# Kernel tuning notes

Hardware: AMD Instinct MI355X
Metric: run time of the kernel (lower is better)

The kernel has to match this reference:

```python
import jax, jax.numpy as jnp
import numpy as np

NBINS_PIX = 256   # uint8 pixel values
NBINS_MEAN = 512  # neighbor mean fits in [0, 408] for side=1


def setup_inputs() -> dict:
    key = jax.random.key(0)
    # uniform [0,1) so x.max() < 1.0 branch (x*255 quantization) is taken, as in the source
    x = jax.random.uniform(key, (64, 1024, 1024), dtype=jnp.float32)
    return {"x": x}


def reference(x):
    H, W = x.shape[-2:]
    x = jax.lax.stop_gradient(x)  # mirrors .clone().detach()
    xf = x.reshape(-1, H, W)
    B = xf.shape[0]
    # quantize: (x*255).to(uint8) if max<1 else x.to(uint8); uint8 cast truncates
    scale = jnp.where(jnp.max(xf) < 1.0, jnp.float32(255.0), jnp.float32(1.0))
    xq = (xf * scale).astype(jnp.uint8).astype(jnp.float32)
    xi = xq.astype(jnp.int32)

    # zero-padded 8-neighbor sum (3x3 window minus center), side=1
    xp = jnp.pad(xi, ((0, 0), (1, 1), (1, 1)))
    nb = jnp.zeros_like(xi)
    for dh in range(3):
        for dw in range(3):
            if dh == 1 and dw == 1:
                continue
            nb = nb + xp[:, dh:dh + H, dw:dw + W]

    # Faithful replication of the source's normalization: the original indexes
    # mean_nb[a, b] where dim0 is the BATCH dim and dim1 is the row dim, so the
    # divisor depends on (batch, row) and broadcasts over columns.
    # t=0: num=3 at 4 (batch,row) corners; then num->5 for edges and interior.
    D = jnp.ones((B, H), dtype=jnp.float32)
    D = D.at[0, 0].set(3.0).at[-1, 0].set(3.0).at[0, -1].set(3.0).at[-1, -1].set(3.0)
    D = D.at[1:-1, 0].set(5.0).at[1:-1, -1].set(5.0)
    D = D.at[0, 1:-1].set(5.0).at[-1, 1:-1].set(5.0)
    D = D.at[1:-1, 1:-1].set(5.0)
    mean_nb = nb.astype(jnp.float32) / D[:, :, None]
    mean_i = mean_nb.astype(jnp.int32)  # trunc toward zero, values >= 0

    # joint (pixel, mean) histogram per image -> entropy, matches unique+counts
    codes = xi * NBINS_MEAN + mean_i  # in [0, 256*512)

    def hist_entropy(c):
        counts = jnp.zeros(NBINS_PIX * NBINS_MEAN, jnp.float32).at[c.reshape(-1)].add(1.0)
        p = counts / (H * W)
        safe = jnp.where(p > 0, p, 1.0)
        return jnp.sum(jnp.where(p > 0, -p * jnp.log2(safe), 0.0))

    ent = jax.vmap(hist_entropy)(codes)  # [B]
    return jnp.mean(ent)
```

## Files before the change

kernel.cpp:

```cpp
#include <hip/hip_runtime.h>

#define IMG_H 1024
#define IMG_W 1024
#define NPIX  (IMG_H * IMG_W)
#define NBINS (256 * 512)
#define TILE  64
#define LW    (TILE + 2)

#define MEANS  428
#define HBINS  (256 * MEANS)
#define HWORDS (HBINS / 4)
#define QUADS  4
#define QROWS  (IMG_H / QUADS)

__global__ __launch_bounds__(1024) void fused_hist_kernel(const float* __restrict__ x,
                                                          unsigned int* __restrict__ partials,
                                                          int B) {
    __shared__ unsigned int h[HWORDS];

    const int blk  = blockIdx.x;
    const int b    = blk >> 2;
    const int quad = blk & 3;
    const int tid  = threadIdx.x;

    for (int i = tid; i < HWORDS; i += 1024) h[i] = 0u;
    __syncthreads();

    const float* img = x + (size_t)b * NPIX;
    const int c0    = (tid & 255) * 4;
    const int strip = tid >> 8;
    const int rs    = quad * QROWS + strip * (QROWS / 4);
    const int re    = rs + QROWS / 4;
    const bool bEdge = (b == 0) || (b == B - 1);

    auto loadraw = [&](int r, float4& f, float& fl, float& fr) {
        if ((unsigned)r < IMG_H) {
            const float* row = img + r * IMG_W;
            f  = *(const float4*)(row + c0);
            fl = (c0 > 0) ? row[c0 - 1] : 0.0f;
            fr = (c0 + 4 < IMG_W) ? row[c0 + 4] : 0.0f;
        } else { f = make_float4(0.f, 0.f, 0.f, 0.f); fl = 0.f; fr = 0.f; }
    };
    auto quant6 = [&](const float4& f, float fl, float fr, int q[6]) {
        q[0] = (int)(fl  * 255.0f);
        q[1] = (int)(f.x * 255.0f);
        q[2] = (int)(f.y * 255.0f);
        q[3] = (int)(f.z * 255.0f);
        q[4] = (int)(f.w * 255.0f);
        q[5] = (int)(fr  * 255.0f);
    };

    int hA[4], hB[4], qB[4];
    {
        float4 f; float fl, fr; loadraw(rs - 1, f, fl, fr);
        int q[6]; quant6(f, fl, fr, q);
#pragma unroll
        for (int i = 0; i < 4; ++i) hA[i] = q[i] + q[i + 1] + q[i + 2];
    }
    {
        float4 f; float fl, fr; loadraw(rs, f, fl, fr);
        int q[6]; quant6(f, fl, fr, q);
#pragma unroll
        for (int i = 0; i < 4; ++i) { hB[i] = q[i] + q[i + 1] + q[i + 2]; qB[i] = q[i + 1]; }
    }
    float4 pf; float pfl, pfr; loadraw(rs + 1, pf, pfl, pfr);

    for (int r = rs; r < re; ++r) {
        float4 cf = pf; float cfl = pfl, cfr = pfr;
        loadraw(r + 2, pf, pfl, pfr);

        int q[6]; quant6(cf, cfl, cfr, q);
        int hC[4];
#pragma unroll
        for (int i = 0; i < 4; ++i) hC[i] = q[i] + q[i + 1] + q[i + 2];

        const bool corner = bEdge && (r == 0 || r == IMG_H - 1);
#pragma unroll
        for (int i = 0; i < 4; ++i) {
            int nb = hA[i] + hB[i] + hC[i] - qB[i];
            unsigned mean = corner ? (unsigned)nb / 3u : (unsigned)nb / 5u;
            unsigned bin  = (unsigned)qB[i] * MEANS + mean;
            atomicAdd(&h[bin >> 2], 1u << ((bin & 3u) * 8u));
            hA[i] = hB[i]; hB[i] = hC[i]; qB[i] = q[i + 1];
        }
    }
    __syncthreads();

    unsigned int* dst = partials + (size_t)blk * HWORDS;
    for (int i = tid; i < HWORDS; i += 1024) dst[i] = h[i];
}

__global__ __launch_bounds__(256) void merge_entropy_kernel(const unsigned int* __restrict__ partials,
                                                            double* __restrict__ acc,
                                                            int B) {
    const int w   = blockIdx.x * 256 + threadIdx.x;
    const int img = blockIdx.y;
    const unsigned int* p = partials + (size_t)img * QUADS * HWORDS + w;
    unsigned w0 = p[0], w1 = p[HWORDS], w2 = p[2 * HWORDS], w3 = p[3 * HWORDS];

    double local = 0.0;
#pragma unroll
    for (int sh = 0; sh < 32; sh += 8) {
        unsigned c = ((w0 >> sh) & 255u) + ((w1 >> sh) & 255u)
                   + ((w2 >> sh) & 255u) + ((w3 >> sh) & 255u);
        if (c) local += (double)c * (20.0 - (double)log2f((float)c));
    }
    for (int off = 32; off > 0; off >>= 1)
        local += __shfl_down(local, off, 64);

    __shared__ double sacc[4];
    const int lane = threadIdx.x & 63;
    const int wid  = threadIdx.x >> 6;
    if (lane == 0) sacc[wid] = local;
    __syncthreads();
    if (threadIdx.x == 0)
        atomicAdd(acc, sacc[0] + sacc[1] + sacc[2] + sacc[3]);
}

__global__ void finalize_kernel(const double* __restrict__ acc,
                                float* __restrict__ out, int B) {
    out[0] = (float)(acc[0] / ((double)NPIX * (double)B));
}

__global__ __launch_bounds__(256) void hist_kernel(const float* __restrict__ x,
                                                   unsigned int* __restrict__ hist,
                                                   int B) {
    __shared__ int s[LW * LW];
    const int tilesPerRow = IMG_W / TILE;
    const int tilesPerImg = (IMG_H / TILE) * tilesPerRow;
    const int b   = blockIdx.x / tilesPerImg;
    const int t   = blockIdx.x % tilesPerImg;
    const int ty0 = (t / tilesPerRow) * TILE;
    const int tx0 = (t % tilesPerRow) * TILE;
    const float* img = x + (size_t)b * NPIX;
    const int tid = threadIdx.x;

    for (int i = tid; i < LW * LW; i += 256) {
        int r = i / LW, c = i - r * LW;
        int gy = ty0 + r - 1, gx = tx0 + c - 1;
        int v = 0;
        if ((unsigned)gy < IMG_H && (unsigned)gx < IMG_W)
            v = (int)(img[gy * IMG_W + gx] * 255.0f);
        s[i] = v;
    }
    __syncthreads();

    unsigned int* hb = hist + (size_t)b * NBINS;
    const bool bEdge = (b == 0) || (b == B - 1);
    const int tx = tid & 63, sy = tid >> 6;
    const int c = tx + 1, r0 = sy * 16;

    int h0, h1, m1;
    { int a = s[r0 * LW + c - 1], m = s[r0 * LW + c], d = s[r0 * LW + c + 1]; h0 = a + m + d; }
    { int a = s[(r0 + 1) * LW + c - 1], m = s[(r0 + 1) * LW + c], d = s[(r0 + 1) * LW + c + 1]; h1 = a + m + d; m1 = m; }

    for (int ry = r0; ry < r0 + 16; ++ry) {
        int a = s[(ry + 2) * LW + c - 1], m = s[(ry + 2) * LW + c], d = s[(ry + 2) * LW + c + 1];
        int h2 = a + m + d;
        int nb = h0 + h1 + h2 - m1;
        int gy = ty0 + ry;
        unsigned mean = (unsigned)nb / 5u;
        if (bEdge && (gy == 0 || gy == IMG_H - 1)) mean = (unsigned)nb / 3u;
        atomicAdd(&hb[m1 * 512 + (int)mean], 1u);
        h0 = h1; h1 = h2; m1 = m;
    }
}

__global__ __launch_bounds__(256) void entropy_kernel(const unsigned int* __restrict__ hist,
                                                      double* __restrict__ acc, int n) {
    double local = 0.0;
    const int stride = gridDim.x * 256;
    for (int i = blockIdx.x * 256 + threadIdx.x; i < n; i += stride) {
        unsigned int cv = hist[i];
        if (cv) local += (double)cv * (20.0 - (double)log2f((float)cv));
    }
    for (int off = 32; off > 0; off >>= 1)
        local += __shfl_down(local, off, 64);
    __shared__ double sacc[4];
    const int lane = threadIdx.x & 63, wid = threadIdx.x >> 6;
    if (lane == 0) sacc[wid] = local;
    __syncthreads();
    if (threadIdx.x == 0)
        atomicAdd(acc, sacc[0] + sacc[1] + sacc[2] + sacc[3]);
}

extern "C" void kernel_launch(void* const* d_in, const int* in_sizes, int n_in,
                              void* d_out, int out_size, void* d_ws, size_t ws_size,
                              hipStream_t stream) {
    const float* x = (const float*)d_in[0];
    const int B = in_sizes[0] / NPIX;

    const size_t partBytes = (size_t)B * QUADS * HWORDS * sizeof(unsigned int);

    if (ws_size >= partBytes + 64) {
        unsigned int* partials = (unsigned int*)d_ws;
        double* acc = (double*)((char*)d_ws + partBytes);
        hipMemsetAsync(acc, 0, sizeof(double), stream);

        fused_hist_kernel<<<B * QUADS, 1024, 0, stream>>>(x, partials, B);
        merge_entropy_kernel<<<dim3(HWORDS / 256, B), 256, 0, stream>>>(partials, acc, B);
        finalize_kernel<<<1, 1, 0, stream>>>(acc, (float*)d_out, B);
    } else {
        unsigned int* hist = (unsigned int*)d_ws;
        const size_t histBytes = (size_t)B * NBINS * sizeof(unsigned int);
        double* acc = (double*)((char*)d_ws + histBytes);
        hipMemsetAsync(d_ws, 0, histBytes + sizeof(double), stream);

        const int tilesPerImg = (IMG_H / TILE) * (IMG_W / TILE);
        hist_kernel<<<B * tilesPerImg, 256, 0, stream>>>(x, hist, B);
        entropy_kernel<<<1024, 256, 0, stream>>>(hist, acc, B * NBINS);
        finalize_kernel<<<1, 1, 0, stream>>>(acc, (float*)d_out, B);
    }
}
```

Baseline: 454.6 us.

## Shrink LDS histogram to a mean window with global spill, split images eight ways

The per-block shared histogram now covers only the central window of neighbor-mean values. The rare out-of-window bins go to a per-image global spill histogram through global atomics. This cuts the per-block LDS footprint so two 1024-thread blocks can share a CU, and each image is split across eight blocks instead of four. In exchange it adds a memset of the spill buffer, an extra entropy kernel over it, and a merge that reads twice as many partials.

```diff
diff --git a/kernel.cpp b/kernel.cpp
--- a/kernel.cpp
+++ b/kernel.cpp
@@ -7,30 +7,35 @@
 #define TILE  64
 #define LW    (TILE + 2)
 
-#define MEANS  428
-#define HBINS  (256 * MEANS)
-#define HWORDS (HBINS / 4)
-#define QUADS  4
-#define QROWS  (IMG_H / QUADS)
-
-__global__ __launch_bounds__(1024) void fused_hist_kernel(const float* __restrict__ x,
-                                                          unsigned int* __restrict__ partials,
-                                                          int B) {
-    __shared__ unsigned int h[HWORDS];
-
-    const int blk  = blockIdx.x;
-    const int b    = blk >> 2;
-    const int quad = blk & 3;
-    const int tid  = threadIdx.x;
-
-    for (int i = tid; i < HWORDS; i += 1024) h[i] = 0u;
+#define WW       316
+#define WM0      45
+#define WBINS    (256 * WW)
+#define WWORDS   (WBINS / 4)
+#define FULLBINS (256 * 426)
+#define OCTS     8
+#define OROWS    (IMG_H / OCTS)
+#define TROWS    (OROWS / 4)
+
+__global__ __launch_bounds__(1024, 8) void fused_hist_kernel(const float* __restrict__ x,
+                                                             unsigned int* __restrict__ partials,
+                                                             unsigned int* __restrict__ spill,
+                                                             int B) {
+    __shared__ unsigned int h[WWORDS];
+
+    const int blk = blockIdx.x;
+    const int b   = blk >> 3;
+    const int oct = blk & 7;
+    const int tid = threadIdx.x;
+
+    for (int i = tid; i < WWORDS; i += 1024) h[i] = 0u;
     __syncthreads();
 
     const float* img = x + (size_t)b * NPIX;
+    unsigned int* sp = spill + (size_t)b * FULLBINS;
     const int c0    = (tid & 255) * 4;
     const int strip = tid >> 8;
-    const int rs    = quad * QROWS + strip * (QROWS / 4);
-    const int re    = rs + QROWS / 4;
+    const int rs    = oct * OROWS + strip * TROWS;
+    const int re    = rs + TROWS;
     const bool bEdge = (b == 0) || (b == B - 1);
 
     auto loadraw = [&](int r, float4& f, float& fl, float& fr) {
@@ -79,31 +84,66 @@
         for (int i = 0; i < 4; ++i) {
             int nb = hA[i] + hB[i] + hC[i] - qB[i];
             unsigned mean = corner ? (unsigned)nb / 3u : (unsigned)nb / 5u;
-            unsigned bin  = (unsigned)qB[i] * MEANS + mean;
-            atomicAdd(&h[bin >> 2], 1u << ((bin & 3u) * 8u));
+            int w = (int)mean - WM0;
+            if ((unsigned)w < (unsigned)WW) {
+                unsigned bin = (unsigned)qB[i] * WW + (unsigned)w;
+                atomicAdd(&h[bin >> 2], 1u << ((bin & 3u) * 8u));
+            } else {
+                atomicAdd(&sp[(unsigned)qB[i] * 426u + mean], 1u);
+            }
             hA[i] = hB[i]; hB[i] = hC[i]; qB[i] = q[i + 1];
         }
     }
     __syncthreads();
 
-    unsigned int* dst = partials + (size_t)blk * HWORDS;
-    for (int i = tid; i < HWORDS; i += 1024) dst[i] = h[i];
-}
-
-__global__ __launch_bounds__(256) void merge_entropy_kernel(const unsigned int* __restrict__ partials,
+    unsigned int* dst = partials + (size_t)blk * WWORDS;
+    for (int i = tid; i < WWORDS; i += 1024) dst[i] = h[i];
+}
+
+__global__ __launch_bounds__(256) void merge_window_kernel(const unsigned int* __restrict__ partials,
+                                                           double* __restrict__ acc,
+                                                           int B) {
+    const int w   = blockIdx.x * 256 + threadIdx.x;
+    const int img = blockIdx.y;
+    const unsigned int* p = partials + (size_t)img * OCTS * WWORDS + w;
+
+    unsigned s0 = p[0],          s1 = p[WWORDS],     s2 = p[2 * WWORDS], s3 = p[3 * WWORDS];
+    unsigned s4 = p[4 * WWORDS], s5 = p[5 * WWORDS], s6 = p[6 * WWORDS], s7 = p[7 * WWORDS];
+
+    double local = 0.0;
+#pragma unroll
+    for (int sh = 0; sh < 32; sh += 8) {
+        unsigned c = ((s0 >> sh) & 255u) + ((s1 >> sh) & 255u)
+                   + ((s2 >> sh) & 255u) + ((s3 >> sh) & 255u)
+                   + ((s4 >> sh) & 255u) + ((s5 >> sh) & 255u)
+                   + ((s6 >> sh) & 255u) + ((s7 >> sh) & 255u);
+        if (c) local += (double)c * (20.0 - (double)log2f((float)c));
+    }
+    for (int off = 32; off > 0; off >>= 1)
+        local += __shfl_down(local, off, 64);
+
+    __shared__ double sacc[4];
+    const int lane = threadIdx.x & 63;
+    const int wid  = threadIdx.x >> 6;
+    if (lane == 0) sacc[wid] = local;
+    __syncthreads();
+    if (threadIdx.x == 0)
+        atomicAdd(acc, sacc[0] + sacc[1] + sacc[2] + sacc[3]);
+}
+
+__global__ __launch_bounds__(256) void spill_entropy_kernel(const unsigned int* __restrict__ spill,
                                                             double* __restrict__ acc,
                                                             int B) {
-    const int w   = blockIdx.x * 256 + threadIdx.x;
+    const int i   = blockIdx.x * 256 + threadIdx.x;
     const int img = blockIdx.y;
-    const unsigned int* p = partials + (size_t)img * QUADS * HWORDS + w;
-    unsigned w0 = p[0], w1 = p[HWORDS], w2 = p[2 * HWORDS], w3 = p[3 * HWORDS];
 
     double local = 0.0;
-#pragma unroll
-    for (int sh = 0; sh < 32; sh += 8) {
-        unsigned c = ((w0 >> sh) & 255u) + ((w1 >> sh) & 255u)
-                   + ((w2 >> sh) & 255u) + ((w3 >> sh) & 255u);
-        if (c) local += (double)c * (20.0 - (double)log2f((float)c));
+    if (i < FULLBINS / 4) {
+        uint4 s = ((const uint4*)(spill + (size_t)img * FULLBINS))[i];
+        if (s.x) local += (double)s.x * (20.0 - (double)log2f((float)s.x));
+        if (s.y) local += (double)s.y * (20.0 - (double)log2f((float)s.y));
+        if (s.z) local += (double)s.z * (20.0 - (double)log2f((float)s.z));
+        if (s.w) local += (double)s.w * (20.0 - (double)log2f((float)s.w));
     }
     for (int off = 32; off > 0; off >>= 1)
         local += __shfl_down(local, off, 64);
@@ -190,15 +230,19 @@
     const float* x = (const float*)d_in[0];
     const int B = in_sizes[0] / NPIX;
 
-    const size_t partBytes = (size_t)B * QUADS * HWORDS * sizeof(unsigned int);
-
-    if (ws_size >= partBytes + 64) {
+    const size_t partBytes  = (size_t)B * OCTS * WWORDS * sizeof(unsigned int);
+    const size_t spillBytes = (size_t)B * FULLBINS * sizeof(unsigned int);
+
+    if (ws_size >= partBytes + spillBytes + 64) {
         unsigned int* partials = (unsigned int*)d_ws;
-        double* acc = (double*)((char*)d_ws + partBytes);
-        hipMemsetAsync(acc, 0, sizeof(double), stream);
-
-        fused_hist_kernel<<<B * QUADS, 1024, 0, stream>>>(x, partials, B);
-        merge_entropy_kernel<<<dim3(HWORDS / 256, B), 256, 0, stream>>>(partials, acc, B);
+        unsigned int* spill    = (unsigned int*)((char*)d_ws + partBytes);
+        double* acc            = (double*)((char*)d_ws + partBytes + spillBytes);
+
+        hipMemsetAsync(spill, 0, spillBytes + sizeof(double), stream);
+
+        fused_hist_kernel<<<B * OCTS, 1024, 0, stream>>>(x, partials, spill, B);
+        merge_window_kernel<<<dim3(WWORDS / 256, B), 256, 0, stream>>>(partials, acc, B);
+        spill_entropy_kernel<<<dim3((FULLBINS / 4 + 255) / 256, B), 256, 0, stream>>>(spill, acc, B);
         finalize_kernel<<<1, 1, 0, stream>>>(acc, (float*)d_out, B);
     } else {
         unsigned int* hist = (unsigned int*)d_ws;
```

Measured after the change: 530.8 us. +16.7%, slower.
